# Optimization experiments

Measured on AMD Instinct MI355X. Metric: run time of the kernel, lower is better.

The kernel has to match this reference:

```python
import jax, jax.numpy as jnp
import numpy as np

NOISE_STD = 0.1

def setup_inputs() -> dict:
    key = jax.random.key(0)
    k1, k2, k3, k4 = jax.random.split(key, 4)
    B, S, D, E, NS = 4, 4096, 2048, 64, 10
    x = jax.random.normal(k1, (B, S, D), dtype=jnp.float32)
    W = jax.random.normal(k2, (E, D), dtype=jnp.float32) * (1.0 / np.sqrt(D))
    scale_condition = jax.random.normal(k3, (NS, 1, 1), dtype=jnp.float32)
    noise = jax.random.normal(k4, (B, S, E), dtype=jnp.float32)
    return {"x": x, "W": W, "scale_condition": scale_condition, "noise": noise, "scale_idx": 3}

def reference(x, W, scale_condition, noise, scale_idx):
    TOP_K = 2
    E = W.shape[0]
    # scale modulation: scale_condition[scale_idx] has shape [1,1], broadcasts over [B,S,D]
    scale_factor = scale_condition[scale_idx]
    router_input = x * (1.0 + scale_factor * 0.1)
    # small GEMM: [B,S,D] x [D,E] -> [B,S,E]
    router_logits = jnp.einsum('bsd,ed->bse', router_input, W)
    router_logits = router_logits + noise * NOISE_STD
    routing_probs = jax.nn.softmax(router_logits, axis=-1)
    routing_weights, selected_experts = jax.lax.top_k(routing_probs, TOP_K)
    routing_weights = routing_weights / jnp.sum(routing_weights, axis=-1, keepdims=True)
    # scatter top-k normalized weights into dense [B,S,E] dispatch tensor
    dispatch_tensor = jnp.sum(
        jax.nn.one_hot(selected_experts, E, dtype=routing_weights.dtype)
        * routing_weights[..., None],
        axis=-2,
    )
    return dispatch_tensor, routing_probs, selected_experts
```

## Files before the change

kernel.cpp:

```cpp
#include <hip/hip_runtime.h>
#include <math.h>

#define D        2048
#define E        64
#define NROWS    16384

#define ROWS_PB  32
#define BKC      64
#define NCH      (D / BKC)
#define XOFF     0
#define WHOFF    8192
#define WLOFF    16384
#define BUFB     24576

#define LSCALE   2048.0f
#define S1       4.8828125e-4f
#define S2       2.384185791015625e-7f

typedef __attribute__((ext_vector_type(8))) _Float16 f16x8;
typedef __attribute__((ext_vector_type(4))) float f32x4;

__device__ __attribute__((aligned(16))) unsigned short g_whi[(size_t)E * D];
__device__ __attribute__((aligned(16))) unsigned short g_wlo[(size_t)E * D];

__device__ __forceinline__ unsigned short f2h(float f) {
    union { _Float16 h; unsigned short u; } c;
    c.h = (_Float16)f;
    return c.u;
}
__device__ __forceinline__ float h2f(unsigned short u) {
    union { _Float16 h; unsigned short u; } c;
    c.u = u;
    return (float)c.h;
}

__device__ __forceinline__ void dma16(const void* g, void* l) {
    __builtin_amdgcn_global_load_lds(
        (const __attribute__((address_space(1))) unsigned int*)g,
        (__attribute__((address_space(3))) unsigned int*)l,
        16, 0, 0);
}

__device__ __forceinline__ void split8(float4 A, float4 B, float f,
                                       f16x8& hi, f16x8& lo) {
    float v[8] = {A.x * f, A.y * f, A.z * f, A.w * f,
                  B.x * f, B.y * f, B.z * f, B.w * f};
    unsigned int hw[4], lw[4];
#pragma unroll
    for (int j = 0; j < 4; ++j) {
        const unsigned short h0 = f2h(v[2*j]);
        const unsigned short h1 = f2h(v[2*j+1]);
        const unsigned short l0 = f2h((v[2*j]   - h2f(h0)) * LSCALE);
        const unsigned short l1 = f2h((v[2*j+1] - h2f(h1)) * LSCALE);
        hw[j] = (unsigned int)h0 | ((unsigned int)h1 << 16);
        lw[j] = (unsigned int)l0 | ((unsigned int)l1 << 16);
    }
    union { uint4 u; f16x8 h; } ch, cl;
    ch.u = make_uint4(hw[0], hw[1], hw[2], hw[3]); hi = ch.h;
    cl.u = make_uint4(lw[0], lw[1], lw[2], lw[3]); lo = cl.h;
}

__global__ __launch_bounds__(256)
void w_cvt(const float* __restrict__ W)
{
    const int i = (blockIdx.x * 256 + threadIdx.x) << 3;
    const float4 a = *(const float4*)(W + i);
    const float4 b = *(const float4*)(W + i + 4);
    float vv[8] = {a.x, a.y, a.z, a.w, b.x, b.y, b.z, b.w};
    unsigned int hw[4], lw[4];
#pragma unroll
    for (int j = 0; j < 4; ++j) {
        const unsigned short h0 = f2h(vv[2*j]);
        const unsigned short h1 = f2h(vv[2*j+1]);
        const unsigned short l0 = f2h((vv[2*j]   - h2f(h0)) * LSCALE);
        const unsigned short l1 = f2h((vv[2*j+1] - h2f(h1)) * LSCALE);
        hw[j] = (unsigned int)h0 | ((unsigned int)h1 << 16);
        lw[j] = (unsigned int)l0 | ((unsigned int)l1 << 16);
    }
    *(uint4*)(g_whi + i) = make_uint4(hw[0], hw[1], hw[2], hw[3]);
    *(uint4*)(g_wlo + i) = make_uint4(lw[0], lw[1], lw[2], lw[3]);
}

__global__ __launch_bounds__(512, 4)
void moe_fused(const float* __restrict__ x,
               const float* __restrict__ scond,
               const int* __restrict__ sidx,
               const float* __restrict__ noise,
               float* __restrict__ dispatch,
               float* __restrict__ probs,
               float* __restrict__ sel)
{
    __shared__ float4 smem_q[2 * BUFB / 16];
    unsigned char* const sm = (unsigned char*)smem_q;

    const int t = threadIdx.x;
    const int l = t & 63;
    const int w = t >> 6;

    const float factor = 1.0f + 0.1f * scond[sidx[0]];

    const int R  = (w >> 2) << 4;
    const int CB = (w & 3) << 4;
    const int fr = l & 15;
    const int fq = l >> 4;
    const int sw = fr & 7;

    const int rowG0 = blockIdx.x * ROWS_PB;

    const float* xsrc =
        x + (size_t)(rowG0 + (t >> 4)) * D + (((t & 15) ^ ((t >> 4) & 7)) << 2);
    const unsigned short* whsrc =
        g_whi + (size_t)(t >> 3) * D + (((t & 7) ^ ((t >> 3) & 7)) << 3);
    const unsigned short* wlsrc =
        g_wlo + (size_t)(t >> 3) * D + (((t & 7) ^ ((t >> 3) & 7)) << 3);

    const int wb = w << 10;

    f32x4 acch = {0.f,0.f,0.f,0.f};
    f32x4 accm = {0.f,0.f,0.f,0.f};
    f32x4 accl = {0.f,0.f,0.f,0.f};

#define STAGE(B, CC) do { \
    unsigned char* const bb_ = sm + (B) * BUFB; \
    dma16(xsrc  + (size_t)(CC) * BKC, bb_ + XOFF  + wb); \
    dma16(whsrc + (size_t)(CC) * BKC, bb_ + WHOFF + wb); \
    dma16(wlsrc + (size_t)(CC) * BKC, bb_ + WLOFF + wb); \
} while (0)

    STAGE(0, 0);
    asm volatile("s_waitcnt vmcnt(0)" ::: "memory");
    __syncthreads();

    for (int c = 0; c < NCH; ++c) {
        const int cur = c & 1;
        if (c + 1 < NCH) STAGE(cur ^ 1, c + 1);

        const unsigned char* bb = sm + cur * BUFB;
        const float* xb = (const float*)(bb + XOFF);
        const unsigned short* whb = (const unsigned short*)(bb + WHOFF);
        const unsigned short* wlb = (const unsigned short*)(bb + WLOFF);

#pragma unroll
        for (int ks = 0; ks < 2; ++ks) {
            const int ls0 = (ks << 3) + (fq << 1);
            const float4 xa = *(const float4*)(xb + ((R + fr) << 6) + ((ls0 ^ sw) << 2));
            const float4 xv = *(const float4*)(xb + ((R + fr) << 6) + (((ls0 + 1) ^ sw) << 2));
            f16x8 ah, al;
            split8(xa, xv, factor, ah, al);
            const int lw_ = (ks << 2) + fq;
            const f16x8 bh = *(const f16x8*)(whb + ((CB + fr) << 6) + ((lw_ ^ sw) << 3));
            const f16x8 bl = *(const f16x8*)(wlb + ((CB + fr) << 6) + ((lw_ ^ sw) << 3));
            acch = __builtin_amdgcn_mfma_f32_16x16x32_f16(ah, bh, acch, 0, 0, 0);
            accm = __builtin_amdgcn_mfma_f32_16x16x32_f16(ah, bl, accm, 0, 0, 0);
            accm = __builtin_amdgcn_mfma_f32_16x16x32_f16(al, bh, accm, 0, 0, 0);
            accl = __builtin_amdgcn_mfma_f32_16x16x32_f16(al, bl, accl, 0, 0, 0);
        }

        __syncthreads();
    }
#undef STAGE

    float* lg = (float*)sm;
#pragma unroll
    for (int j = 0; j < 4; ++j) {
        const int rr = R + (fq << 2) + j;
        lg[rr * 68 + CB + fr] = acch[j] + S1 * accm[j] + S2 * accl[j];
    }
    __syncthreads();

    const int r0 = w << 2;
#pragma unroll
    for (int i = 0; i < 4; ++i) {
        const int G = rowG0 + r0 + i;
        const float v = lg[(r0 + i) * 68 + l] + 0.1f * noise[(size_t)G * E + l];

        float m = v;
#pragma unroll
        for (int off = 32; off > 0; off >>= 1)
            m = fmaxf(m, __shfl_xor(m, off, 64));
        const float p = expf(v - m);
        float s = p;
#pragma unroll
        for (int off = 32; off > 0; off >>= 1)
            s += __shfl_xor(s, off, 64);
        const float prob = p / s;
        probs[(size_t)G * E + l] = prob;

        float bv = prob; int bi = l;
#pragma unroll
        for (int off = 32; off > 0; off >>= 1) {
            const float ov = __shfl_xor(bv, off, 64);
            const int   oi = __shfl_xor(bi, off, 64);
            if (ov > bv || (ov == bv && oi < bi)) { bv = ov; bi = oi; }
        }
        float cv = (l == bi) ? -INFINITY : prob;
        int ci = l;
#pragma unroll
        for (int off = 32; off > 0; off >>= 1) {
            const float ov = __shfl_xor(cv, off, 64);
            const int   oi = __shfl_xor(ci, off, 64);
            if (ov > cv || (ov == cv && oi < ci)) { cv = ov; ci = oi; }
        }

        const float sum2 = bv + cv;
        float dval = 0.f;
        if (l == bi) dval = bv / sum2;
        if (l == ci) dval = cv / sum2;
        dispatch[(size_t)G * E + l] = dval;

        if (l == 0) {
            float2 sv; sv.x = (float)bi; sv.y = (float)ci;
            *(float2*)(sel + (size_t)G * 2) = sv;
        }
    }
}

extern "C" void kernel_launch(void* const* d_in, const int* in_sizes, int n_in,
                              void* d_out, int out_size, void* d_ws, size_t ws_size,
                              hipStream_t stream) {
    const float* x     = (const float*)d_in[0];
    const float* W     = (const float*)d_in[1];
    const float* scond = (const float*)d_in[2];
    const float* noise = (const float*)d_in[3];
    const int*   sidx  = (const int*)d_in[4];

    float* out      = (float*)d_out;
    float* dispatch = out;
    float* probs    = out + (size_t)NROWS * E;
    float* sel      = out + 2 * (size_t)NROWS * E;

    (void)d_ws; (void)ws_size;

    w_cvt<<<dim3(64), dim3(256), 0, stream>>>(W);
    moe_fused<<<dim3(NROWS / ROWS_PB), dim3(512), 0, stream>>>(
        x, scond, sidx, noise, dispatch, probs, sel);
}
```

Measured before the change: 224.5 us.

## Load W hi/lo straight to registers and deepen the x LDS ring to four buffers

The split-fp16 weight tiles are no longer staged through LDS. Each wave now reads its B fragments directly from global memory, where they are small and L2-resident, into registers each chunk. The x tile alone uses a four-slot LDS ring with prefetch distance two. This leaves one barrier per iteration instead of a wait-plus-barrier pair, and cuts LDS capacity and traffic. In exchange, every chunk exposes L2 latency on the weight loads just before the MFMAs, and correctness depends on the vmcnt(1) accounting matching the order of the global loads.

```diff
diff --git a/kernel.cpp b/kernel.cpp
--- a/kernel.cpp
+++ b/kernel.cpp
@@ -8,10 +8,8 @@
 #define ROWS_PB  32
 #define BKC      64
 #define NCH      (D / BKC)
-#define XOFF     0
-#define WHOFF    8192
-#define WLOFF    16384
-#define BUFB     24576
+#define XBUFB    8192
+#define NBUF     4
 
 #define LSCALE   2048.0f
 #define S1       4.8828125e-4f
@@ -32,6 +30,12 @@
     union { _Float16 h; unsigned short u; } c;
     c.u = u;
     return (float)c.h;
+}
+
+__device__ __forceinline__ f16x8 ld_b16(const unsigned short* p) {
+    union { uint4 u; f16x8 h; } c;
+    c.u = *(const uint4*)p;
+    return c.h;
 }
 
 __device__ __forceinline__ void dma16(const void* g, void* l) {
@@ -90,7 +94,7 @@
                float* __restrict__ probs,
                float* __restrict__ sel)
 {
-    __shared__ float4 smem_q[2 * BUFB / 16];
+    __shared__ float4 smem_q[NBUF * XBUFB / 16];
     unsigned char* const sm = (unsigned char*)smem_q;
 
     const int t = threadIdx.x;
@@ -109,37 +113,33 @@
 
     const float* xsrc =
         x + (size_t)(rowG0 + (t >> 4)) * D + (((t & 15) ^ ((t >> 4) & 7)) << 2);
-    const unsigned short* whsrc =
-        g_whi + (size_t)(t >> 3) * D + (((t & 7) ^ ((t >> 3) & 7)) << 3);
-    const unsigned short* wlsrc =
-        g_wlo + (size_t)(t >> 3) * D + (((t & 7) ^ ((t >> 3) & 7)) << 3);
-
     const int wb = w << 10;
+
+    const unsigned short* whb = g_whi + (size_t)(CB + fr) * D + (fq << 3);
+    const unsigned short* wlb = g_wlo + (size_t)(CB + fr) * D + (fq << 3);
 
     f32x4 acch = {0.f,0.f,0.f,0.f};
     f32x4 accm = {0.f,0.f,0.f,0.f};
     f32x4 accl = {0.f,0.f,0.f,0.f};
 
-#define STAGE(B, CC) do { \
-    unsigned char* const bb_ = sm + (B) * BUFB; \
-    dma16(xsrc  + (size_t)(CC) * BKC, bb_ + XOFF  + wb); \
-    dma16(whsrc + (size_t)(CC) * BKC, bb_ + WHOFF + wb); \
-    dma16(wlsrc + (size_t)(CC) * BKC, bb_ + WLOFF + wb); \
-} while (0)
-
-    STAGE(0, 0);
-    asm volatile("s_waitcnt vmcnt(0)" ::: "memory");
-    __syncthreads();
+    dma16(xsrc,            sm + 0 * XBUFB + wb);
+    dma16(xsrc + 1 * BKC,  sm + 1 * XBUFB + wb);
 
     for (int c = 0; c < NCH; ++c) {
-        const int cur = c & 1;
-        if (c + 1 < NCH) STAGE(cur ^ 1, c + 1);
-
-        const unsigned char* bb = sm + cur * BUFB;
-        const float* xb = (const float*)(bb + XOFF);
-        const unsigned short* whb = (const unsigned short*)(bb + WHOFF);
-        const unsigned short* wlb = (const unsigned short*)(bb + WLOFF);
-
+        asm volatile("s_waitcnt vmcnt(1)" ::: "memory");
+        __builtin_amdgcn_s_barrier();
+
+        const int kc = c * BKC;
+        const f16x8 bh0 = ld_b16(whb + kc);
+        const f16x8 bl0 = ld_b16(wlb + kc);
+        const f16x8 bh1 = ld_b16(whb + kc + 32);
+        const f16x8 bl1 = ld_b16(wlb + kc + 32);
+        __builtin_amdgcn_sched_barrier(0);
+
+        if (c + 2 < NCH)
+            dma16(xsrc + (size_t)(c + 2) * BKC, sm + ((c + 2) & 3) * XBUFB + wb);
+
+        const float* xb = (const float*)(sm + (c & 3) * XBUFB);
 #pragma unroll
         for (int ks = 0; ks < 2; ++ks) {
             const int ls0 = (ks << 3) + (fq << 1);
@@ -147,18 +147,16 @@
             const float4 xv = *(const float4*)(xb + ((R + fr) << 6) + (((ls0 + 1) ^ sw) << 2));
             f16x8 ah, al;
             split8(xa, xv, factor, ah, al);
-            const int lw_ = (ks << 2) + fq;
-            const f16x8 bh = *(const f16x8*)(whb + ((CB + fr) << 6) + ((lw_ ^ sw) << 3));
-            const f16x8 bl = *(const f16x8*)(wlb + ((CB + fr) << 6) + ((lw_ ^ sw) << 3));
+            const f16x8 bh = ks ? bh1 : bh0;
+            const f16x8 bl = ks ? bl1 : bl0;
             acch = __builtin_amdgcn_mfma_f32_16x16x32_f16(ah, bh, acch, 0, 0, 0);
             accm = __builtin_amdgcn_mfma_f32_16x16x32_f16(ah, bl, accm, 0, 0, 0);
             accm = __builtin_amdgcn_mfma_f32_16x16x32_f16(al, bh, accm, 0, 0, 0);
             accl = __builtin_amdgcn_mfma_f32_16x16x32_f16(al, bl, accl, 0, 0, 0);
         }
-
-        __syncthreads();
-    }
-#undef STAGE
+    }
+
+    __syncthreads();
 
     float* lg = (float*)sm;
 #pragma unroll
```

After: 262.9 us. +17.1%, slower.
